# Optimization experiments

Measured on AMD Instinct MI355X. Metric: run time of the kernel, lower is better.

## Reference

```python
import jax, jax.numpy as jnp
import numpy as np

B, N, DIM, H, DH = 2, 2048, 512, 8, 64
EPS = 1e-3  # eps added after relu feature map, per original


def setup_inputs() -> dict:
    key = jax.random.key(0)
    k0, k1, k2, k3, k4 = jax.random.split(key, 5)
    s_in = 1.0 / np.sqrt(DIM)
    s_out = 1.0 / np.sqrt(H * DH)
    return {
        "x": jax.random.normal(k0, (B, N, DIM), jnp.float32),
        "Wq": jax.random.normal(k1, (DIM, H * DH), jnp.float32) * s_in,
        "Wk": jax.random.normal(k2, (DIM, H * DH), jnp.float32) * s_in,
        "Wv": jax.random.normal(k3, (DIM, H * DH), jnp.float32) * s_in,
        "Wo": jax.random.normal(k4, (H * DH, DIM), jnp.float32) * s_out,
        "bo": jnp.zeros((DIM,), jnp.float32),
    }


def causal_linear_attn(q, k, v, eps=EPS):
    # bucket_size == 1 path of the original causal_linear_attn (blindspot_size=1):
    # relu feature map + eps, running cumsums of k and of the outer product k v^T.
    q = jax.nn.relu(q) + eps
    k = jax.nn.relu(k) + eps
    k_cum = jnp.cumsum(k, axis=2)                                  # [b,h,n,d]
    ctx = jnp.cumsum(k[..., :, None] * v[..., None, :], axis=2)    # [b,h,n,d,e]
    d_inv = 1.0 / jnp.einsum('bhnd,bhnd->bhn', q, k_cum)           # [b,h,n]
    return jnp.einsum('bhnd,bhnde,bhn->bhne', q, ctx, d_inv)       # [b,h,n,e]


def reference(x, Wq, Wk, Wv, Wo, bo):
    b, n, _ = x.shape
    split = lambda t: t.reshape(b, n, H, DH).transpose(0, 2, 1, 3)  # [b,h,n,dh]
    q = split(x @ Wq)
    k = split(x @ Wk)
    v = split(x @ Wv)
    out = causal_linear_attn(q, k, v)
    out = out.transpose(0, 2, 1, 3).reshape(b, n, H * DH)
    return out @ Wo + bo
```

## Files before the change

### kernel.cpp

```cpp
#include <hip/hip_runtime.h>

constexpr int kB   = 2;
constexpr int kN   = 2048;
constexpr int kDIM = 512;
constexpr int kH   = 8;
constexpr int kDH  = 64;
constexpr int kBH  = kB * kH;
constexpr int NROWS = kB * kN;
constexpr int CHUNK = 64;
constexpr int NCH   = kN / CHUNK;
constexpr int CBSTRIDE = kDH * kDH + kDH;
constexpr float kEPS = 1e-3f;

typedef _Float16 f16x8 __attribute__((ext_vector_type(8)));
typedef _Float16 f16x4 __attribute__((ext_vector_type(4)));
typedef float    floatx4 __attribute__((ext_vector_type(4)));

__device__ __forceinline__ void async_copy16(void* lds, const void* g) {
    __builtin_amdgcn_global_load_lds(
        (const __attribute__((address_space(1))) void*)g,
        (__attribute__((address_space(3))) void*)lds,
        16, 0, 0);
}

__global__ __launch_bounds__(256)
void prep_kernel(const float* __restrict__ Wq, const float* __restrict__ Wk,
                 const float* __restrict__ Wv, const float* __restrict__ Wo,
                 const float* __restrict__ x,
                 _Float16* __restrict__ WT, _Float16* __restrict__ WoT,
                 _Float16* __restrict__ xh)
{
    const int z = blockIdx.z;
    if (z >= 4) {
        const size_t base = (((size_t)(z - 4) * 256 + blockIdx.y * 16 + blockIdx.x) * 256 +
                             threadIdx.x) * 4;
        const float4 a = *(const float4*)(x + base);
        f16x4 o;
        o[0] = (_Float16)a.x; o[1] = (_Float16)a.y;
        o[2] = (_Float16)a.z; o[3] = (_Float16)a.w;
        *(f16x4*)(xh + base) = o;
        return;
    }
    __shared__ float tile[32][33];
    const float* src = (z == 0) ? Wq : (z == 1) ? Wk : (z == 2) ? Wv : Wo;
    _Float16* dst = (z < 3) ? (WT + (size_t)z * 512 * 512) : WoT;
    const int r0 = blockIdx.y * 32, c0 = blockIdx.x * 32;
    const int tr = threadIdx.x >> 5, tc = threadIdx.x & 31;
    #pragma unroll
    for (int i = 0; i < 4; ++i)
        tile[tr + 8 * i][tc] = src[(size_t)(r0 + tr + 8 * i) * 512 + c0 + tc];
    __syncthreads();
    #pragma unroll
    for (int i = 0; i < 4; ++i)
        dst[(size_t)(c0 + tr + 8 * i) * 512 + r0 + tc] = (_Float16)tile[tc][tr + 8 * i];
}

__global__ __launch_bounds__(512)
void qkv_gemm_kernel(const _Float16* __restrict__ A,
                     const _Float16* __restrict__ BT,
                     _Float16* __restrict__ qh,
                     _Float16* __restrict__ khb,
                     _Float16* __restrict__ kTh,
                     _Float16* __restrict__ vTh)
{
    constexpr int K = 512;
    __shared__ _Float16 As[128 * 64];
    __shared__ _Float16 Bs[256 * 64];

    const int t = threadIdx.x;
    const int l = t & 63;
    const int w = t >> 6;
    const int wm = w >> 2, wn = w & 3;
    const int m0 = blockIdx.y * 128;
    const int n0 = blockIdx.x * 256;

    const int r15 = l & 15, kq = l >> 4, sw = r15 & 7;

    floatx4 acc[4][4];
    #pragma unroll
    for (int mi = 0; mi < 4; ++mi)
        #pragma unroll
        for (int ni = 0; ni < 4; ++ni)
            acc[mi][ni] = (floatx4){0.f, 0.f, 0.f, 0.f};

    const char* Abase = (const char*)(A + (size_t)m0 * K);
    const char* Bbase = (const char*)(BT + (size_t)n0 * K);
    char* AsB = (char*)As;
    char* BsB = (char*)Bs;

    const char* ArdB = (const char*)As + (wm * 64 + r15) * 128;
    const char* BrdB = (const char*)Bs + (wn * 64 + r15) * 128;
    const int sw0 = ((kq ^ sw) << 4);
    const int sw1 = (((4 + kq) ^ sw) << 4);

    for (int k0 = 0; k0 < K; k0 += 64) {
        #pragma unroll
        for (int i = 0; i < 2; ++i) {
            const int s = i * 512 + t;
            const int row = s >> 3, sl = s & 7;
            const int gsl = sl ^ (row & 7);
            async_copy16(AsB + row * 128 + sl * 16,
                         Abase + (size_t)row * (K * 2) + k0 * 2 + gsl * 16);
        }
        #pragma unroll
        for (int i = 0; i < 4; ++i) {
            const int s = i * 512 + t;
            const int row = s >> 3, sl = s & 7;
            const int gsl = sl ^ (row & 7);
            async_copy16(BsB + row * 128 + sl * 16,
                         Bbase + (size_t)row * (K * 2) + k0 * 2 + gsl * 16);
        }
        __syncthreads();

        f16x8 af[4][2], bf[4][2];
        #pragma unroll
        for (int i = 0; i < 4; ++i) {
            af[i][0] = *(const f16x8*)(ArdB + i * 2048 + sw0);
            af[i][1] = *(const f16x8*)(ArdB + i * 2048 + sw1);
            bf[i][0] = *(const f16x8*)(BrdB + i * 2048 + sw0);
            bf[i][1] = *(const f16x8*)(BrdB + i * 2048 + sw1);
        }
        #pragma unroll
        for (int kk = 0; kk < 2; ++kk)
            #pragma unroll
            for (int mi = 0; mi < 4; ++mi)
                #pragma unroll
                for (int ni = 0; ni < 4; ++ni)
                    acc[mi][ni] = __builtin_amdgcn_mfma_f32_16x16x32_f16(
                        af[mi][kk], bf[ni][kk], acc[mi][ni], 0, 0, 0);
        __syncthreads();
    }

    #pragma unroll
    for (int ni = 0; ni < 4; ++ni) {
        const int col = n0 + wn * 64 + ni * 16 + r15;
        const int which = col >> 9;
        const int h = (col >> 6) & 7, e = col & 63;
        #pragma unroll
        for (int mi = 0; mi < 4; ++mi) {
            const int row0 = m0 + wm * 64 + mi * 16 + kq * 4;
            const int b = row0 >> 11, nn = row0 & 2047;
            const int bh = b * 8 + h;
            float vv[4];
            #pragma unroll
            for (int r = 0; r < 4; ++r) {
                float v = acc[mi][ni][r];
                if (which < 2) v = fmaxf(v, 0.f) + kEPS;
                vv[r] = v;
            }
            if (which == 0) {
                #pragma unroll
                for (int r = 0; r < 4; ++r)
                    qh[((size_t)bh * kN + nn + r) * 64 + e] = (_Float16)vv[r];
            } else if (which == 1) {
                #pragma unroll
                for (int r = 0; r < 4; ++r)
                    khb[((size_t)bh * kN + nn + r) * 64 + e] = (_Float16)vv[r];
                f16x4 t4;
                t4[0] = (_Float16)vv[0]; t4[1] = (_Float16)vv[1];
                t4[2] = (_Float16)vv[2]; t4[3] = (_Float16)vv[3];
                *(f16x4*)(kTh + ((size_t)bh * 64 + e) * kN + nn) = t4;
            } else {
                f16x4 t4;
                t4[0] = (_Float16)vv[0]; t4[1] = (_Float16)vv[1];
                t4[2] = (_Float16)vv[2]; t4[3] = (_Float16)vv[3];
                *(f16x4*)(vTh + ((size_t)bh * 64 + e) * kN + nn) = t4;
            }
        }
    }
}

__global__ __launch_bounds__(256)
void chunk_sum_kernel(const _Float16* __restrict__ kTh, const _Float16* __restrict__ vTh,
                      float* __restrict__ cbuf)
{
    const int ch = blockIdx.x, bh = blockIdx.y;
    const int t = threadIdx.x, l = t & 63, w = t >> 6;
    const int r15 = l & 15, kq = l >> 4;

    const _Float16* vbase = vTh + (size_t)bh * 64 * kN + ch * 64;
    const _Float16* kbase = kTh + (size_t)bh * 64 * kN + ch * 64;

    f16x8 av[2], bk[4][2];
    #pragma unroll
    for (int kk = 0; kk < 2; ++kk) {
        av[kk] = *(const f16x8*)(vbase + (size_t)(w * 16 + r15) * kN + kk * 32 + kq * 8);
        #pragma unroll
        for (int ni = 0; ni < 4; ++ni)
            bk[ni][kk] = *(const f16x8*)(kbase + (size_t)(ni * 16 + r15) * kN + kk * 32 + kq * 8);
    }
    floatx4 acc[4];
    #pragma unroll
    for (int ni = 0; ni < 4; ++ni) acc[ni] = (floatx4){0.f, 0.f, 0.f, 0.f};
    #pragma unroll
    for (int kk = 0; kk < 2; ++kk)
        #pragma unroll
        for (int ni = 0; ni < 4; ++ni)
            acc[ni] = __builtin_amdgcn_mfma_f32_16x16x32_f16(av[kk], bk[ni][kk], acc[ni], 0, 0, 0);

    float* out = cbuf + ((size_t)bh * NCH + ch) * CBSTRIDE;
    #pragma unroll
    for (int ni = 0; ni < 4; ++ni)
        #pragma unroll
        for (int r = 0; r < 4; ++r)
            out[(size_t)(w * 16 + kq * 4 + r) * 64 + ni * 16 + r15] = acc[ni][r];

    if (t < 64) {
        const _Float16* kp = kbase + (size_t)t * kN;
        float z = 0.f;
        #pragma unroll
        for (int j = 0; j < 8; ++j) {
            f16x8 v8 = *(const f16x8*)(kp + j * 8);
            #pragma unroll
            for (int u = 0; u < 8; ++u) z += (float)v8[u];
        }
        out[4096 + t] = z;
    }
}

__global__ __launch_bounds__(256)
void prefix_kernel(const float* __restrict__ cbuf, _Float16* __restrict__ spre16,
                   float* __restrict__ zpre)
{
    const int bh = blockIdx.y;
    const int i = blockIdx.x * 256 + threadIdx.x;
    if (i >= CBSTRIDE) return;
    const float* src = cbuf + (size_t)bh * NCH * CBSTRIDE + i;
    _Float16* dst = spre16 + (size_t)bh * NCH * CBSTRIDE + i;
    float* zp = zpre + (size_t)bh * NCH * 64;
    const bool isz = (i >= 4096);
    float vals[NCH];
    #pragma unroll
    for (int c = 0; c < NCH; ++c) vals[c] = src[(size_t)c * CBSTRIDE];
    float a = 0.f;
    #pragma unroll
    for (int c = 0; c < NCH; ++c) {
        dst[(size_t)c * CBSTRIDE] = (_Float16)a;
        if (isz) zp[c * 64 + (i - 4096)] = a;
        a += vals[c];
    }
}

__global__ __launch_bounds__(256)
void chunk_out_kernel(const _Float16* __restrict__ qh, const _Float16* __restrict__ khb,
                      const _Float16* __restrict__ vTh, const _Float16* __restrict__ spre16,
                      const float* __restrict__ zpre, _Float16* __restrict__ attnh)
{
    const int ch = blockIdx.x, bh = blockIdx.y;
    const int t = threadIdx.x, l = t & 63, w = t >> 6;
    const int r15 = l & 15, kq = l >> 4;

    __shared__ _Float16 Plds[64 * 64];
    __shared__ float denp[64];
    __shared__ float denf[64];

    const size_t rowbase = (size_t)bh * kN + ch * 64;

    f16x8 aq[2], bk[4][2];
    #pragma unroll
    for (int kk = 0; kk < 2; ++kk) {
        aq[kk] = *(const f16x8*)(qh + (rowbase + w * 16 + r15) * 64 + kk * 32 + kq * 8);
        #pragma unroll
        for (int ni = 0; ni < 4; ++ni)
            bk[ni][kk] = *(const f16x8*)(khb + (rowbase + ni * 16 + r15) * 64 + kk * 32 + kq * 8);
    }
    floatx4 sacc[4];
    #pragma unroll
    for (int ni = 0; ni < 4; ++ni) sacc[ni] = (floatx4){0.f, 0.f, 0.f, 0.f};
    #pragma unroll
    for (int kk = 0; kk < 2; ++kk)
        #pragma unroll
        for (int ni = 0; ni < 4; ++ni)
            sacc[ni] = __builtin_amdgcn_mfma_f32_16x16x32_f16(aq[kk], bk[ni][kk], sacc[ni], 0, 0, 0);

    const int qrow = w * 16 + kq * 4;
    float psum[4] = {0.f, 0.f, 0.f, 0.f};
    #pragma unroll
    for (int ni = 0; ni < 4; ++ni) {
        const int m = ni * 16 + r15;
        #pragma unroll
        for (int r = 0; r < 4; ++r) {
            const int row = qrow + r;
            const float v = (m <= row) ? sacc[ni][r] : 0.f;
            psum[r] += v;
            const int byte = row * 128 + ((((unsigned)m >> 3) ^ (row & 7)) << 4) + (m & 7) * 2;
            *(_Float16*)((char*)Plds + byte) = (_Float16)v;
        }
    }
    #pragma unroll
    for (int r = 0; r < 4; ++r) {
        float p = psum[r];
        p += __shfl_xor(p, 1, 16);
        p += __shfl_xor(p, 2, 16);
        p += __shfl_xor(p, 4, 16);
        p += __shfl_xor(p, 8, 16);
        if (r15 == 0) denp[qrow + r] = p;
    }
    __syncthreads();

    if (t < 64) {
        const _Float16* qp = qh + (rowbase + t) * 64;
        const float* zp = zpre + ((size_t)bh * NCH + ch) * 64;
        float s = denp[t];
        #pragma unroll
        for (int j = 0; j < 8; ++j) {
            f16x8 q8 = *(const f16x8*)(qp + j * 8);
            #pragma unroll
            for (int u = 0; u < 8; ++u) s += (float)q8[u] * zp[j * 8 + u];
        }
        denf[t] = 1.0f / s;
    }

    f16x8 ap[2], bv[4][2], bs[4][2];
    #pragma unroll
    for (int km = 0; km < 2; ++km)
        ap[km] = *(const f16x8*)((char*)Plds + (w * 16 + r15) * 128 +
                                 (((km * 4 + kq) ^ (r15 & 7)) << 4));
    #pragma unroll
    for (int ni = 0; ni < 4; ++ni) {
        #pragma unroll
        for (int km = 0; km < 2; ++km)
            bv[ni][km] = *(const f16x8*)(vTh + ((size_t)bh * 64 + ni * 16 + r15) * kN +
                                         ch * 64 + km * 32 + kq * 8);
    }
    const _Float16* sp = spre16 + ((size_t)bh * NCH + ch) * CBSTRIDE;
    #pragma unroll
    for (int ni = 0; ni < 4; ++ni)
        #pragma unroll
        for (int kd = 0; kd < 2; ++kd)
            bs[ni][kd] = *(const f16x8*)(sp + (size_t)(ni * 16 + r15) * 64 + kd * 32 + kq * 8);

    floatx4 oacc[4];
    #pragma unroll
    for (int ni = 0; ni < 4; ++ni) oacc[ni] = (floatx4){0.f, 0.f, 0.f, 0.f};
    #pragma unroll
    for (int km = 0; km < 2; ++km)
        #pragma unroll
        for (int ni = 0; ni < 4; ++ni)
            oacc[ni] = __builtin_amdgcn_mfma_f32_16x16x32_f16(ap[km], bv[ni][km], oacc[ni], 0, 0, 0);
    #pragma unroll
    for (int kd = 0; kd < 2; ++kd)
        #pragma unroll
        for (int ni = 0; ni < 4; ++ni)
            oacc[ni] = __builtin_amdgcn_mfma_f32_16x16x32_f16(aq[kd], bs[ni][kd], oacc[ni], 0, 0, 0);
    __syncthreads();

    const int b = bh >> 3, h = bh & 7;
    #pragma unroll
    for (int ni = 0; ni < 4; ++ni) {
        const int e = ni * 16 + r15;
        #pragma unroll
        for (int r = 0; r < 4; ++r) {
            const int qn = qrow + r;
            const float ov = oacc[ni][r] * denf[qn];
            attnh[((size_t)(b * kN + ch * 64 + qn)) * 512 + h * 64 + e] = (_Float16)ov;
        }
    }
}

__global__ __launch_bounds__(256)
void out_gemm_kernel(const _Float16* __restrict__ A,
                     const _Float16* __restrict__ BT,
                     const float* __restrict__ bo,
                     float* __restrict__ outf)
{
    constexpr int K = 512;
    __shared__ _Float16 As[128 * 64];
    __shared__ _Float16 Bs[128 * 64];

    const int t = threadIdx.x;
    const int l = t & 63;
    const int w = t >> 6;
    const int wm = w >> 1, wn = w & 1;
    const int m0 = blockIdx.y * 128;
    const int n0 = blockIdx.x * 128;

    const int r15 = l & 15, kq = l >> 4, sw = r15 & 7;

    floatx4 acc[4][4];
    #pragma unroll
    for (int mi = 0; mi < 4; ++mi)
        #pragma unroll
        for (int ni = 0; ni < 4; ++ni)
            acc[mi][ni] = (floatx4){0.f, 0.f, 0.f, 0.f};

    const int srow  = t >> 3;
    const int sslot = t & 7;

    const char* Abase = (const char*)(A + (size_t)m0 * K);
    const char* Bbase = (const char*)(BT + (size_t)n0 * K);
    char* AsB = (char*)As;
    char* BsB = (char*)Bs;

    const char* ArdB = (const char*)As + (wm * 64 + r15) * 128;
    const char* BrdB = (const char*)Bs + (wn * 64 + r15) * 128;
    const int sw0 = ((kq ^ sw) << 4);
    const int sw1 = (((4 + kq) ^ sw) << 4);

    for (int k0 = 0; k0 < K; k0 += 64) {
        #pragma unroll
        for (int i = 0; i < 4; ++i) {
            const int row = i * 32 + srow;
            const int gsl = sslot ^ (row & 7);
            async_copy16(AsB + row * 128 + sslot * 16,
                         Abase + (size_t)row * (K * 2) + k0 * 2 + gsl * 16);
            async_copy16(BsB + row * 128 + sslot * 16,
                         Bbase + (size_t)row * (K * 2) + k0 * 2 + gsl * 16);
        }
        __syncthreads();

        f16x8 af[4][2], bf[4][2];
        #pragma unroll
        for (int i = 0; i < 4; ++i) {
            af[i][0] = *(const f16x8*)(ArdB + i * 2048 + sw0);
            af[i][1] = *(const f16x8*)(ArdB + i * 2048 + sw1);
            bf[i][0] = *(const f16x8*)(BrdB + i * 2048 + sw0);
            bf[i][1] = *(const f16x8*)(BrdB + i * 2048 + sw1);
        }
        #pragma unroll
        for (int kk = 0; kk < 2; ++kk)
            #pragma unroll
            for (int mi = 0; mi < 4; ++mi)
                #pragma unroll
                for (int ni = 0; ni < 4; ++ni)
                    acc[mi][ni] = __builtin_amdgcn_mfma_f32_16x16x32_f16(
                        af[mi][kk], bf[ni][kk], acc[mi][ni], 0, 0, 0);
        __syncthreads();
    }

    #pragma unroll
    for (int ni = 0; ni < 4; ++ni) {
        const int col = n0 + wn * 64 + ni * 16 + r15;
        const float bias = bo[col];
        #pragma unroll
        for (int mi = 0; mi < 4; ++mi) {
            const int row = m0 + wm * 64 + mi * 16 + kq * 4;
            #pragma unroll
            for (int r = 0; r < 4; ++r)
                outf[(size_t)(row + r) * 512 + col] = acc[mi][ni][r] + bias;
        }
    }
}

extern "C" void kernel_launch(void* const* d_in, const int* in_sizes, int n_in,
                              void* d_out, int out_size, void* d_ws, size_t ws_size,
                              hipStream_t stream)
{
    const float* x  = (const float*)d_in[0];
    const float* Wq = (const float*)d_in[1];
    const float* Wk = (const float*)d_in[2];
    const float* Wv = (const float*)d_in[3];
    const float* Wo = (const float*)d_in[4];
    const float* bo = (const float*)d_in[5];
    float* out = (float*)d_out;

    char* ws = (char*)d_ws;
    _Float16* qh     = (_Float16*)(ws + 0);
    _Float16* khb    = (_Float16*)(ws + 4194304);
    _Float16* kTh    = (_Float16*)(ws + 8388608);
    _Float16* vTh    = (_Float16*)(ws + 12582912);
    float*    cbuf   = (float*)(ws + 16777216);
    _Float16* spre16 = (_Float16*)(ws + 25296896);
    float*    zpre   = (float*)(ws + 29556736);
    _Float16* WT     = (_Float16*)(ws + 29687808);
    _Float16* WoT    = (_Float16*)(ws + 31260672);
    _Float16* attnh  = (_Float16*)(ws + 31784960);
    _Float16* xh     = (_Float16*)(ws + 35979264);

    prep_kernel<<<dim3(16, 16, 12), 256, 0, stream>>>(Wq, Wk, Wv, Wo, x, WT, WoT, xh);
    qkv_gemm_kernel<<<dim3(6, NROWS / 128), 512, 0, stream>>>(
        xh, WT, qh, khb, kTh, vTh);
    chunk_sum_kernel<<<dim3(NCH, kBH), 256, 0, stream>>>(kTh, vTh, cbuf);
    prefix_kernel<<<dim3(17, kBH), 256, 0, stream>>>(cbuf, spre16, zpre);
    chunk_out_kernel<<<dim3(NCH, kBH), 256, 0, stream>>>(
        qh, khb, vTh, spre16, zpre, attnh);
    out_gemm_kernel<<<dim3(4, NROWS / 128), 256, 0, stream>>>(
        attnh, WoT, bo, out);
}
```

Baseline: 58.07 us.

## Fuse chunk-sum and prefix kernels into a sequential MFMA scan kernel

Replaces the per-chunk KV outer-product kernel and the separate prefix-sum kernel with one scan kernel. Each block owns one (bh, half of dh) tile and walks all chunks in order, keeping the running state in MFMA accumulators and writing the exclusive prefix straight to the fp16 buffer. The key sums are now computed with an MFMA against a vector of ones. This removes the fp32 intermediate buffer round trip and one launch, but cuts parallelism to 32 blocks that each run a serial 32-step loop, so latency may dominate.

```diff
diff --git a/kernel.cpp b/kernel.cpp
--- a/kernel.cpp
+++ b/kernel.cpp
@@ -171,73 +171,63 @@
 }
 
 __global__ __launch_bounds__(256)
-void chunk_sum_kernel(const _Float16* __restrict__ kTh, const _Float16* __restrict__ vTh,
-                      float* __restrict__ cbuf)
-{
-    const int ch = blockIdx.x, bh = blockIdx.y;
+void scan_kernel(const _Float16* __restrict__ kTh, const _Float16* __restrict__ vTh,
+                 _Float16* __restrict__ spre16, float* __restrict__ zpre)
+{
+    const int dh = blockIdx.x;
+    const int bh = blockIdx.y;
     const int t = threadIdx.x, l = t & 63, w = t >> 6;
     const int r15 = l & 15, kq = l >> 4;
 
-    const _Float16* vbase = vTh + (size_t)bh * 64 * kN + ch * 64;
-    const _Float16* kbase = kTh + (size_t)bh * 64 * kN + ch * 64;
-
-    f16x8 av[2], bk[4][2];
-    #pragma unroll
-    for (int kk = 0; kk < 2; ++kk) {
-        av[kk] = *(const f16x8*)(vbase + (size_t)(w * 16 + r15) * kN + kk * 32 + kq * 8);
-        #pragma unroll
-        for (int ni = 0; ni < 4; ++ni)
-            bk[ni][kk] = *(const f16x8*)(kbase + (size_t)(ni * 16 + r15) * kN + kk * 32 + kq * 8);
-    }
-    floatx4 acc[4];
-    #pragma unroll
-    for (int ni = 0; ni < 4; ++ni) acc[ni] = (floatx4){0.f, 0.f, 0.f, 0.f};
-    #pragma unroll
-    for (int kk = 0; kk < 2; ++kk)
-        #pragma unroll
-        for (int ni = 0; ni < 4; ++ni)
-            acc[ni] = __builtin_amdgcn_mfma_f32_16x16x32_f16(av[kk], bk[ni][kk], acc[ni], 0, 0, 0);
-
-    float* out = cbuf + ((size_t)bh * NCH + ch) * CBSTRIDE;
-    #pragma unroll
-    for (int ni = 0; ni < 4; ++ni)
-        #pragma unroll
-        for (int r = 0; r < 4; ++r)
-            out[(size_t)(w * 16 + kq * 4 + r) * 64 + ni * 16 + r15] = acc[ni][r];
-
-    if (t < 64) {
-        const _Float16* kp = kbase + (size_t)t * kN;
-        float z = 0.f;
-        #pragma unroll
-        for (int j = 0; j < 8; ++j) {
-            f16x8 v8 = *(const f16x8*)(kp + j * 8);
-            #pragma unroll
-            for (int u = 0; u < 8; ++u) z += (float)v8[u];
-        }
-        out[4096 + t] = z;
-    }
-}
-
-__global__ __launch_bounds__(256)
-void prefix_kernel(const float* __restrict__ cbuf, _Float16* __restrict__ spre16,
-                   float* __restrict__ zpre)
-{
-    const int bh = blockIdx.y;
-    const int i = blockIdx.x * 256 + threadIdx.x;
-    if (i >= CBSTRIDE) return;
-    const float* src = cbuf + (size_t)bh * NCH * CBSTRIDE + i;
-    _Float16* dst = spre16 + (size_t)bh * NCH * CBSTRIDE + i;
-    float* zp = zpre + (size_t)bh * NCH * 64;
-    const bool isz = (i >= 4096);
-    float vals[NCH];
-    #pragma unroll
-    for (int c = 0; c < NCH; ++c) vals[c] = src[(size_t)c * CBSTRIDE];
-    float a = 0.f;
-    #pragma unroll
-    for (int c = 0; c < NCH; ++c) {
-        dst[(size_t)c * CBSTRIDE] = (_Float16)a;
-        if (isz) zp[c * 64 + (i - 4096)] = a;
-        a += vals[c];
+    const _Float16* vbase = vTh + (size_t)bh * 64 * kN;
+    const _Float16* kbase = kTh + (size_t)bh * 64 * kN;
+
+    floatx4 acc[2];
+    acc[0] = (floatx4){0.f, 0.f, 0.f, 0.f};
+    acc[1] = (floatx4){0.f, 0.f, 0.f, 0.f};
+    floatx4 zacc[2];
+    zacc[0] = (floatx4){0.f, 0.f, 0.f, 0.f};
+    zacc[1] = (floatx4){0.f, 0.f, 0.f, 0.f};
+
+    f16x8 ones;
+    #pragma unroll
+    for (int u = 0; u < 8; ++u) ones[u] = (_Float16)1.0f;
+
+    for (int ch = 0; ch < NCH; ++ch) {
+        _Float16* sp = spre16 + ((size_t)bh * NCH + ch) * CBSTRIDE;
+        #pragma unroll
+        for (int ni = 0; ni < 2; ++ni)
+            #pragma unroll
+            for (int r = 0; r < 4; ++r)
+                sp[(size_t)(w * 16 + kq * 4 + r) * 64 + dh * 32 + ni * 16 + r15] =
+                    (_Float16)acc[ni][r];
+        if (w == 0 && kq == 0) {
+            float* zp = zpre + ((size_t)bh * NCH + ch) * 64 + dh * 32;
+            zp[r15]      = zacc[0][0];
+            zp[16 + r15] = zacc[1][0];
+        }
+        f16x8 av[2], bk[2][2];
+        #pragma unroll
+        for (int kk = 0; kk < 2; ++kk) {
+            av[kk] = *(const f16x8*)(vbase + (size_t)(w * 16 + r15) * kN +
+                                     ch * 64 + kk * 32 + kq * 8);
+            #pragma unroll
+            for (int ni = 0; ni < 2; ++ni)
+                bk[ni][kk] = *(const f16x8*)(kbase + (size_t)(dh * 32 + ni * 16 + r15) * kN +
+                                             ch * 64 + kk * 32 + kq * 8);
+        }
+        #pragma unroll
+        for (int kk = 0; kk < 2; ++kk)
+            #pragma unroll
+            for (int ni = 0; ni < 2; ++ni)
+                acc[ni] = __builtin_amdgcn_mfma_f32_16x16x32_f16(av[kk], bk[ni][kk], acc[ni], 0, 0, 0);
+        if (w == 0) {
+            #pragma unroll
+            for (int kk = 0; kk < 2; ++kk)
+                #pragma unroll
+                for (int ni = 0; ni < 2; ++ni)
+                    zacc[ni] = __builtin_amdgcn_mfma_f32_16x16x32_f16(ones, bk[ni][kk], zacc[ni], 0, 0, 0);
+        }
     }
 }
 
@@ -459,19 +449,17 @@
     _Float16* khb    = (_Float16*)(ws + 4194304);
     _Float16* kTh    = (_Float16*)(ws + 8388608);
     _Float16* vTh    = (_Float16*)(ws + 12582912);
-    float*    cbuf   = (float*)(ws + 16777216);
-    _Float16* spre16 = (_Float16*)(ws + 25296896);
-    float*    zpre   = (float*)(ws + 29556736);
-    _Float16* WT     = (_Float16*)(ws + 29687808);
-    _Float16* WoT    = (_Float16*)(ws + 31260672);
-    _Float16* attnh  = (_Float16*)(ws + 31784960);
-    _Float16* xh     = (_Float16*)(ws + 35979264);
+    _Float16* spre16 = (_Float16*)(ws + 16777216);
+    float*    zpre   = (float*)(ws + 21037056);
+    _Float16* WT     = (_Float16*)(ws + 21168128);
+    _Float16* WoT    = (_Float16*)(ws + 22740992);
+    _Float16* attnh  = (_Float16*)(ws + 23265280);
+    _Float16* xh     = (_Float16*)(ws + 27459584);
 
     prep_kernel<<<dim3(16, 16, 12), 256, 0, stream>>>(Wq, Wk, Wv, Wo, x, WT, WoT, xh);
     qkv_gemm_kernel<<<dim3(6, NROWS / 128), 512, 0, stream>>>(
         xh, WT, qh, khb, kTh, vTh);
-    chunk_sum_kernel<<<dim3(NCH, kBH), 256, 0, stream>>>(kTh, vTh, cbuf);
-    prefix_kernel<<<dim3(17, kBH), 256, 0, stream>>>(cbuf, spre16, zpre);
+    scan_kernel<<<dim3(2, kBH), 256, 0, stream>>>(kTh, vTh, spre16, zpre);
     chunk_out_kernel<<<dim3(NCH, kBH), 256, 0, stream>>>(
         qh, khb, vTh, spre16, zpre, attnh);
     out_gemm_kernel<<<dim3(4, NROWS / 128), 256, 0, stream>>>(
```

Result: slower. 73.31 us (+26.2%).

## Fold chunk prefix scan into chunk_out kernel and store chunk sums in fp16

Applied to the files above, without the earlier changes.

Removes the separate prefix_kernel launch. Each chunk_out block now sums all earlier chunk KV summaries itself and stages the result in swizzled LDS, where it is used as the MFMA B operand. Chunk sums are written in fp16 instead of fp32, which halves that traffic and cuts one kernel launch plus the round trip through global memory. In exchange the redundant work grows quadratically with chunk index: the last chunks read up to 31 summaries each. The per-chunk fp16 rounding before summation may also cost some accuracy.

```diff
diff --git a/kernel.cpp b/kernel.cpp
--- a/kernel.cpp
+++ b/kernel.cpp
@@ -9,7 +9,6 @@
 constexpr int NROWS = kB * kN;
 constexpr int CHUNK = 64;
 constexpr int NCH   = kN / CHUNK;
-constexpr int CBSTRIDE = kDH * kDH + kDH;
 constexpr float kEPS = 1e-3f;
 
 typedef _Float16 f16x8 __attribute__((ext_vector_type(8)));
@@ -172,7 +171,7 @@
 
 __global__ __launch_bounds__(256)
 void chunk_sum_kernel(const _Float16* __restrict__ kTh, const _Float16* __restrict__ vTh,
-                      float* __restrict__ cbuf)
+                      _Float16* __restrict__ csum16, float* __restrict__ zsum)
 {
     const int ch = blockIdx.x, bh = blockIdx.y;
     const int t = threadIdx.x, l = t & 63, w = t >> 6;
@@ -198,12 +197,12 @@
         for (int ni = 0; ni < 4; ++ni)
             acc[ni] = __builtin_amdgcn_mfma_f32_16x16x32_f16(av[kk], bk[ni][kk], acc[ni], 0, 0, 0);
 
-    float* out = cbuf + ((size_t)bh * NCH + ch) * CBSTRIDE;
+    _Float16* out = csum16 + ((size_t)bh * NCH + ch) * 4096;
     #pragma unroll
     for (int ni = 0; ni < 4; ++ni)
         #pragma unroll
         for (int r = 0; r < 4; ++r)
-            out[(size_t)(w * 16 + kq * 4 + r) * 64 + ni * 16 + r15] = acc[ni][r];
+            out[(size_t)(w * 16 + kq * 4 + r) * 64 + ni * 16 + r15] = (_Float16)acc[ni][r];
 
     if (t < 64) {
         const _Float16* kp = kbase + (size_t)t * kN;
@@ -214,45 +213,50 @@
             #pragma unroll
             for (int u = 0; u < 8; ++u) z += (float)v8[u];
         }
-        out[4096 + t] = z;
-    }
-}
-
-__global__ __launch_bounds__(256)
-void prefix_kernel(const float* __restrict__ cbuf, _Float16* __restrict__ spre16,
-                   float* __restrict__ zpre)
-{
-    const int bh = blockIdx.y;
-    const int i = blockIdx.x * 256 + threadIdx.x;
-    if (i >= CBSTRIDE) return;
-    const float* src = cbuf + (size_t)bh * NCH * CBSTRIDE + i;
-    _Float16* dst = spre16 + (size_t)bh * NCH * CBSTRIDE + i;
-    float* zp = zpre + (size_t)bh * NCH * 64;
-    const bool isz = (i >= 4096);
-    float vals[NCH];
-    #pragma unroll
-    for (int c = 0; c < NCH; ++c) vals[c] = src[(size_t)c * CBSTRIDE];
-    float a = 0.f;
-    #pragma unroll
-    for (int c = 0; c < NCH; ++c) {
-        dst[(size_t)c * CBSTRIDE] = (_Float16)a;
-        if (isz) zp[c * 64 + (i - 4096)] = a;
-        a += vals[c];
+        zsum[((size_t)bh * NCH + ch) * 64 + t] = z;
     }
 }
 
 __global__ __launch_bounds__(256)
 void chunk_out_kernel(const _Float16* __restrict__ qh, const _Float16* __restrict__ khb,
-                      const _Float16* __restrict__ vTh, const _Float16* __restrict__ spre16,
-                      const float* __restrict__ zpre, _Float16* __restrict__ attnh)
+                      const _Float16* __restrict__ vTh, const _Float16* __restrict__ csum16,
+                      const float* __restrict__ zsum, _Float16* __restrict__ attnh)
 {
     const int ch = blockIdx.x, bh = blockIdx.y;
     const int t = threadIdx.x, l = t & 63, w = t >> 6;
     const int r15 = l & 15, kq = l >> 4;
 
     __shared__ _Float16 Plds[64 * 64];
+    __shared__ _Float16 Spre[64 * 64];
+    __shared__ float zprel[64];
     __shared__ float denp[64];
     __shared__ float denf[64];
+
+    {
+        const int e0 = t >> 2;
+        const int sg = (t & 3) * 2;
+        float a0[8] = {}, a1[8] = {};
+        const _Float16* cbase = csum16 + (size_t)bh * NCH * 4096 + e0 * 64 + sg * 8;
+        for (int c = 0; c < ch; ++c) {
+            const _Float16* cp = cbase + (size_t)c * 4096;
+            const f16x8 u0 = *(const f16x8*)(cp);
+            const f16x8 u1 = *(const f16x8*)(cp + 8);
+            #pragma unroll
+            for (int j = 0; j < 8; ++j) { a0[j] += (float)u0[j]; a1[j] += (float)u1[j]; }
+        }
+        f16x8 s0, s1;
+        #pragma unroll
+        for (int j = 0; j < 8; ++j) { s0[j] = (_Float16)a0[j]; s1[j] = (_Float16)a1[j]; }
+        char* SB = (char*)Spre;
+        *(f16x8*)(SB + e0 * 128 + ((sg ^ (e0 & 7)) << 4)) = s0;
+        *(f16x8*)(SB + e0 * 128 + (((sg + 1) ^ (e0 & 7)) << 4)) = s1;
+        if (t < 64) {
+            float z = 0.f;
+            for (int c = 0; c < ch; ++c)
+                z += zsum[((size_t)bh * NCH + c) * 64 + t];
+            zprel[t] = z;
+        }
+    }
 
     const size_t rowbase = (size_t)bh * kN + ch * 64;
 
@@ -300,13 +304,12 @@
 
     if (t < 64) {
         const _Float16* qp = qh + (rowbase + t) * 64;
-        const float* zp = zpre + ((size_t)bh * NCH + ch) * 64;
         float s = denp[t];
         #pragma unroll
         for (int j = 0; j < 8; ++j) {
             f16x8 q8 = *(const f16x8*)(qp + j * 8);
             #pragma unroll
-            for (int u = 0; u < 8; ++u) s += (float)q8[u] * zp[j * 8 + u];
+            for (int u = 0; u < 8; ++u) s += (float)q8[u] * zprel[j * 8 + u];
         }
         denf[t] = 1.0f / s;
     }
@@ -323,12 +326,14 @@
             bv[ni][km] = *(const f16x8*)(vTh + ((size_t)bh * 64 + ni * 16 + r15) * kN +
                                          ch * 64 + km * 32 + kq * 8);
     }
-    const _Float16* sp = spre16 + ((size_t)bh * NCH + ch) * CBSTRIDE;
-    #pragma unroll
-    for (int ni = 0; ni < 4; ++ni)
+    #pragma unroll
+    for (int ni = 0; ni < 4; ++ni) {
+        const int e = ni * 16 + r15;
         #pragma unroll
         for (int kd = 0; kd < 2; ++kd)
-            bs[ni][kd] = *(const f16x8*)(sp + (size_t)(ni * 16 + r15) * 64 + kd * 32 + kq * 8);
+            bs[ni][kd] = *(const f16x8*)((char*)Spre + e * 128 +
+                                         (((kd * 4 + kq) ^ (e & 7)) << 4));
+    }
 
     floatx4 oacc[4];
     #pragma unroll
@@ -459,21 +464,19 @@
     _Float16* khb    = (_Float16*)(ws + 4194304);
     _Float16* kTh    = (_Float16*)(ws + 8388608);
     _Float16* vTh    = (_Float16*)(ws + 12582912);
-    float*    cbuf   = (float*)(ws + 16777216);
-    _Float16* spre16 = (_Float16*)(ws + 25296896);
-    float*    zpre   = (float*)(ws + 29556736);
-    _Float16* WT     = (_Float16*)(ws + 29687808);
-    _Float16* WoT    = (_Float16*)(ws + 31260672);
-    _Float16* attnh  = (_Float16*)(ws + 31784960);
-    _Float16* xh     = (_Float16*)(ws + 35979264);
+    _Float16* csum16 = (_Float16*)(ws + 16777216);
+    float*    zsum   = (float*)(ws + 20971520);
+    _Float16* WT     = (_Float16*)(ws + 21102592);
+    _Float16* WoT    = (_Float16*)(ws + 22675456);
+    _Float16* attnh  = (_Float16*)(ws + 23199744);
+    _Float16* xh     = (_Float16*)(ws + 27394048);
 
     prep_kernel<<<dim3(16, 16, 12), 256, 0, stream>>>(Wq, Wk, Wv, Wo, x, WT, WoT, xh);
     qkv_gemm_kernel<<<dim3(6, NROWS / 128), 512, 0, stream>>>(
         xh, WT, qh, khb, kTh, vTh);
-    chunk_sum_kernel<<<dim3(NCH, kBH), 256, 0, stream>>>(kTh, vTh, cbuf);
-    prefix_kernel<<<dim3(17, kBH), 256, 0, stream>>>(cbuf, spre16, zpre);
+    chunk_sum_kernel<<<dim3(NCH, kBH), 256, 0, stream>>>(kTh, vTh, csum16, zsum);
     chunk_out_kernel<<<dim3(NCH, kBH), 256, 0, stream>>>(
-        qh, khb, vTh, spre16, zpre, attnh);
+        qh, khb, vTh, csum16, zsum, attnh);
     out_gemm_kernel<<<dim3(4, NROWS / 128), 256, 0, stream>>>(
         attnh, WoT, bo, out);
 }
```

After: 66.53 us. +14.6%, slower.
